# Optimization experiments

Measured on AMD Instinct MI355X. Metric: run time of the kernel, lower is better.

Reference implementation:

```python
import jax, jax.numpy as jnp
import numpy as np

N_TASK, N_WORKER, N_STATION = 20000, 5000, 1000
D, HEADS, LAYERS = 64, 4, 2
EDGE_COUNTS = [50000, 30000, 30000, 40000, 40000]
# (n_src, n_dst) per relation: precedes, assigned_to, has_task, can_do, done_by
EDGE_SPEC = [(N_TASK, N_TASK), (N_TASK, N_STATION), (N_STATION, N_TASK), (N_WORKER, N_TASK), (N_TASK, N_WORKER)]
EDGE_TYPES = [('task', 'task'), ('task', 'station'), ('station', 'task'), ('worker', 'task'), ('task', 'worker')]


def setup_inputs() -> dict:
    key = jax.random.key(0)
    ks = iter(jax.random.split(key, 64))
    inp = {}
    inp['x_task'] = jax.random.normal(next(ks), (N_TASK, 16), jnp.float32)
    inp['x_worker'] = jax.random.normal(next(ks), (N_WORKER, 12), jnp.float32)
    inp['x_station'] = jax.random.normal(next(ks), (N_STATION, 10), jnp.float32)
    for i, (E, (ns, nd)) in enumerate(zip(EDGE_COUNTS, EDGE_SPEC)):
        src = jax.random.randint(next(ks), (E,), 0, ns)
        dst = jax.random.randint(next(ks), (E,), 0, nd)
        inp[f'ei{i}'] = jnp.stack([src, dst]).astype(jnp.int32)
    def lin(k, i, o):
        return jax.random.normal(k, (i, o), jnp.float32) / np.float32(np.sqrt(i))
    # feature embedder params (Linear + LayerNorm affine) per node type
    for name, fd in [('task', 16), ('worker', 12), ('station', 10)]:
        inp[f'W_{name}'] = lin(next(ks), fd, D)
        inp[f'b_{name}'] = jnp.zeros((D,), jnp.float32)
        inp[f'g_{name}'] = jnp.ones((D,), jnp.float32)
        inp[f'beta_{name}'] = jnp.zeros((D,), jnp.float32)
    # stacked GATv2 params: [layers, 5 edge types, ...]
    inp['gat_Wl'] = jax.random.normal(next(ks), (LAYERS, 5, D, HEADS * D), jnp.float32) / np.float32(np.sqrt(D))
    inp['gat_Wr'] = jax.random.normal(next(ks), (LAYERS, 5, D, HEADS * D), jnp.float32) / np.float32(np.sqrt(D))
    inp['gat_att'] = jax.random.normal(next(ks), (LAYERS, 5, HEADS, D), jnp.float32) * np.float32(0.1)
    inp['gat_bias'] = jnp.zeros((LAYERS, 5, D), jnp.float32)
    return inp


def _layer_norm(x, g, b):
    m = x.mean(-1, keepdims=True)
    v = ((x - m) ** 2).mean(-1, keepdims=True)
    return (x - m) * jax.lax.rsqrt(v + 1e-5) * g + b


def _gatv2(x_src, x_dst, ei, Wl, Wr, att, bias):
    # GATv2Conv, concat=False (mean over heads), no self loops
    n_dst = x_dst.shape[0]
    xl = (x_src @ Wl).reshape(-1, HEADS, D)  # [Ns,H,Dh]
    xr = (x_dst @ Wr).reshape(-1, HEADS, D)  # [Nd,H,Dh]
    src, dst = ei[0], ei[1]
    e = jax.nn.leaky_relu(xl[src] + xr[dst], 0.2)          # [E,H,Dh]
    logits = jnp.einsum('ehd,hd->eh', e, att)              # [E,H]
    m = jax.ops.segment_max(logits, dst, num_segments=n_dst)
    ex = jnp.exp(logits - m[dst])
    denom = jax.ops.segment_sum(ex, dst, num_segments=n_dst)
    alpha = ex / denom[dst]                                # segment softmax per dst node
    out = jax.ops.segment_sum(alpha[..., None] * xl[src], dst, num_segments=n_dst)
    return out.mean(axis=1) + bias                         # [Nd,D]


def _forward(x_task, x_worker, x_station, eis,
             W_task, b_task, g_task, beta_task,
             W_worker, b_worker, g_worker, beta_worker,
             W_station, b_station, g_station, beta_station,
             gat_Wl, gat_Wr, gat_att, gat_bias):
    x = {
        'task': jax.nn.relu(_layer_norm(x_task @ W_task + b_task, g_task, beta_task)),
        'worker': jax.nn.relu(_layer_norm(x_worker @ W_worker + b_worker, g_worker, beta_worker)),
        'station': jax.nn.relu(_layer_norm(x_station @ W_station + b_station, g_station, beta_station)),
    }
    for l in range(LAYERS):
        agg = {'task': 0.0, 'worker': 0.0, 'station': 0.0}
        for t, (st, dt) in enumerate(EDGE_TYPES):
            agg[dt] = agg[dt] + _gatv2(x[st], x[dt], eis[t], gat_Wl[l, t], gat_Wr[l, t], gat_att[l, t], gat_bias[l, t])
        x = {k: jax.nn.relu(agg[k]) + x[k] for k in x}  # HeteroConv sum aggr, then ReLU + residual
    gc = jnp.concatenate([
        x['station'].mean(0), x['task'].mean(0), x['worker'].mean(0),
        x['station'].max(0), x['task'].max(0), x['worker'].max(0),
    ])[None, :]  # [1, 6*D]
    return x['task'], x['worker'], x['station'], gc


def reference(x_task, x_worker, x_station, ei0, ei1, ei2, ei3, ei4,
              W_task, b_task, g_task, beta_task,
              W_worker, b_worker, g_worker, beta_worker,
              W_station, b_station, g_station, beta_station,
              gat_Wl, gat_Wr, gat_att, gat_bias):
    return _forward(x_task, x_worker, x_station, (ei0, ei1, ei2, ei3, ei4),
                    W_task, b_task, g_task, beta_task,
                    W_worker, b_worker, g_worker, beta_worker,
                    W_station, b_station, g_station, beta_station,
                    gat_Wl, gat_Wr, gat_att, gat_bias)
```

## Files before the change

kernel.cpp:

```cpp
#include <hip/hip_runtime.h>
#include <math.h>

#define NT 20000
#define NW 5000
#define NS 1000

typedef __attribute__((ext_vector_type(8))) short bf16x8;
typedef __attribute__((ext_vector_type(4))) float f32x4;

#define CB_T 1250
#define CB_W 313
#define CB_S 63
#define CB_ALL 1626

struct GemmSeg { const short* X; const short* Wt; short* Y; int N; int blk0; };
struct GemmTab { GemmSeg s[10]; int nseg; };

struct GatTab {
  const int* rowp[5]; const int* col[5];
  const short* xl[5]; const short* xr[5];
  const float* att; const float* bias;
  float* aggT; float* aggW; float* aggS;
};

struct EdgeSeg { const int* ei; int* cnt; int* col; int E; int blk0; };
struct EdgeTab { EdgeSeg s[5]; int nseg; };

struct ScanTab { int* cnt[5]; int* rowp[5]; int n[5]; };

struct Mega0 {
  const float *xT, *xW, *xS, *WT, *WW, *WS;
  const float *bT, *gT, *beT, *bW, *gW, *beW, *bS, *gS, *beS;
  float *yT, *yW, *yS; short *ybT, *ybW, *ybS;
  const float *gWl, *gWr; short *Wlt, *Wrt; int* nxtAll;
};

__device__ __forceinline__ float wsum64(float v) {
  #pragma unroll
  for (int o = 32; o > 0; o >>= 1) v += __shfl_xor(v, o, 64);
  return v;
}
__device__ __forceinline__ short f2b(float f) {
  unsigned u = __float_as_uint(f);
  unsigned r = (u + 0x7FFFu + ((u >> 16) & 1u)) >> 16;
  return (short)(unsigned short)r;
}
__device__ __forceinline__ float blo(unsigned x) { return __uint_as_float(x << 16); }
__device__ __forceinline__ float bhi(unsigned x) { return __uint_as_float(x & 0xFFFF0000u); }

__global__ void mega0_kernel(Mega0 M) {
  int b = blockIdx.x;
  if (b < 6500) {
    int gid = b * 256 + threadIdx.x;
    int wid = gid >> 6, lane = gid & 63;
    const float *x, *W, *bb, *gg, *be; float* y; short* yb; int FD, n;
    if (wid < NT)            { x = M.xT; W = M.WT; bb = M.bT; gg = M.gT; be = M.beT; y = M.yT; yb = M.ybT; FD = 16; n = wid; }
    else if (wid < NT + NW)  { x = M.xW; W = M.WW; bb = M.bW; gg = M.gW; be = M.beW; y = M.yW; yb = M.ybW; FD = 12; n = wid - NT; }
    else                     { x = M.xS; W = M.WS; bb = M.bS; gg = M.gS; be = M.beS; y = M.yS; yb = M.ybS; FD = 10; n = wid - NT - NW; }
    const float* xr = x + (size_t)n * FD;
    float acc = bb[lane];
    for (int k = 0; k < FD; ++k) acc = fmaf(xr[k], W[k * 64 + lane], acc);
    float m = wsum64(acc) * (1.f / 64.f);
    float d = acc - m;
    float v = wsum64(d * d) * (1.f / 64.f);
    float o = d * rsqrtf(v + 1e-5f) * gg[lane] + be[lane];
    o = fmaxf(o, 0.f);
    y[(size_t)n * 64 + lane] = o;
    yb[(size_t)n * 64 + lane] = f2b(o);
  } else {
    int idx = (b - 6500) * 256 + threadIdx.x;
    if (idx < 66000) M.nxtAll[idx] = 0;
    int side = idx >= 163840;
    int j = idx - side * 163840;
    int m = j >> 14, e = j & 16383;
    int k = e >> 8, colv = e & 255;
    const float* src = side ? M.gWr : M.gWl;
    short* dst = side ? M.Wrt : M.Wlt;
    dst[m * 16384 + colv * 64 + k] = f2b(src[m * 16384 + e]);
  }
}

__global__ void count_kernel(EdgeTab tab) {
  int b = blockIdx.x, si = 0;
  for (int i = 1; i < tab.nseg; ++i) if (b >= tab.s[i].blk0) si = i;
  EdgeSeg sg = tab.s[si];
  int e = (b - sg.blk0) * 256 + threadIdx.x;
  if (e < sg.E) atomicAdd(&sg.cnt[sg.ei[sg.E + e]], 1);
}

__global__ void scan_kernel(ScanTab tab) {
  int t = blockIdx.x;
  int* cnt = tab.cnt[t]; int* rowp = tab.rowp[t]; int n = tab.n[t];
  __shared__ int wsums[16];
  __shared__ int carry_s;
  int tid = threadIdx.x, lane = tid & 63, w = tid >> 6;
  if (tid == 0) carry_s = 0;
  __syncthreads();
  for (int base = 0; base < n; base += 1024) {
    int i = base + tid;
    int v = (i < n) ? cnt[i] : 0;
    int s = v;
    #pragma unroll
    for (int o = 1; o < 64; o <<= 1) { int x = __shfl_up(s, o, 64); if (lane >= o) s += x; }
    if (lane == 63) wsums[w] = s;
    __syncthreads();
    if (w == 0 && lane < 16) {
      int x = wsums[lane];
      #pragma unroll
      for (int o = 1; o < 16; o <<= 1) { int y = __shfl_up(x, o, 16); if (lane >= o) x += y; }
      wsums[lane] = x;
    }
    __syncthreads();
    int carry   = carry_s;
    int waveoff = (w == 0) ? 0 : wsums[w - 1];
    int exc     = carry + waveoff + s - v;
    if (i < n) { rowp[i] = exc; cnt[i] = exc; }
    __syncthreads();
    if (tid == 0) carry_s += wsums[15];
    __syncthreads();
  }
  if (threadIdx.x == 0) rowp[n] = carry_s;
}

__global__ void fill_kernel(EdgeTab tab) {
  int b = blockIdx.x, si = 0;
  for (int i = 1; i < tab.nseg; ++i) if (b >= tab.s[i].blk0) si = i;
  EdgeSeg sg = tab.s[si];
  int e = (b - sg.blk0) * 256 + threadIdx.x;
  if (e >= sg.E) return;
  int s = sg.ei[e], d = sg.ei[sg.E + e];
  int pos = atomicAdd(&sg.cnt[d], 1);
  sg.col[pos] = s;
}

__global__ __launch_bounds__(256) void gemm_kernel(GemmTab tab) {
  __shared__ short lds[4096 + 16896];
  int b = blockIdx.x, si = 0;
  for (int i = 1; i < tab.nseg; ++i) if (b >= tab.s[i].blk0) si = i;
  GemmSeg sg = tab.s[si];
  int r0 = (b - sg.blk0) * 64;
  int tid = threadIdx.x;
  #pragma unroll
  for (int it = 0; it < 2; ++it) {
    int idx = it * 256 + tid;
    int row = idx >> 3, kq = idx & 7;
    bf16x8 v = {0, 0, 0, 0, 0, 0, 0, 0};
    if (r0 + row < sg.N) v = *(const bf16x8*)&sg.X[(size_t)(r0 + row) * 64 + kq * 8];
    *(bf16x8*)&lds[(row * 8 + (kq ^ (row & 7))) * 8] = v;
  }
  #pragma unroll
  for (int it = 0; it < 8; ++it) {
    int idx = it * 256 + tid;
    int col = idx >> 3, kq = idx & 7;
    bf16x8 v = *(const bf16x8*)&sg.Wt[col * 64 + kq * 8];
    *(bf16x8*)&lds[4096 + (col * 8 + (kq ^ (col & 7))) * 8] = v;
  }
  __syncthreads();
  int lane = tid & 63, wv = tid >> 6;
  int r = lane & 15, hk = lane >> 4;
  f32x4 acc[4][4];
  #pragma unroll
  for (int rt = 0; rt < 4; ++rt)
    #pragma unroll
    for (int ct = 0; ct < 4; ++ct) acc[rt][ct] = (f32x4){0.f, 0.f, 0.f, 0.f};
  #pragma unroll
  for (int kk = 0; kk < 2; ++kk) {
    int kq = kk * 4 + hk;
    bf16x8 a[4], bb[4];
    #pragma unroll
    for (int rt = 0; rt < 4; ++rt) {
      int row = rt * 16 + r;
      a[rt] = *(const bf16x8*)&lds[(row * 8 + (kq ^ (row & 7))) * 8];
    }
    #pragma unroll
    for (int ct = 0; ct < 4; ++ct) {
      int col = wv * 64 + ct * 16 + r;
      bb[ct] = *(const bf16x8*)&lds[4096 + (col * 8 + (kq ^ (col & 7))) * 8];
    }
    #pragma unroll
    for (int rt = 0; rt < 4; ++rt)
      #pragma unroll
      for (int ct = 0; ct < 4; ++ct)
        acc[rt][ct] = __builtin_amdgcn_mfma_f32_16x16x32_bf16(a[rt], bb[ct], acc[rt][ct], 0, 0, 0);
  }
  __syncthreads();
  #pragma unroll
  for (int rt = 0; rt < 4; ++rt)
    #pragma unroll
    for (int j = 0; j < 4; ++j) {
      int rowl = rt * 16 + hk * 4 + j;
      #pragma unroll
      for (int ct = 0; ct < 4; ++ct)
        lds[rowl * 264 + wv * 64 + ct * 16 + r] = f2b(acc[rt][ct][j]);
    }
  __syncthreads();
  #pragma unroll
  for (int it = 0; it < 8; ++it) {
    int idx = it * 256 + tid;
    int row = idx >> 5, v8 = idx & 31;
    if (r0 + row < sg.N) {
      bf16x8 v = *(const bf16x8*)&lds[row * 264 + v8 * 8];
      *(bf16x8*)&sg.Y[(size_t)(r0 + row) * 256 + v8 * 8] = v;
    }
  }
}

__global__ void gat_kernel(GatTab tab) {
  int gwave = (blockIdx.x * blockDim.x + threadIdx.x) >> 6;
  int lane  = threadIdx.x & 63;
  int h = lane >> 4, lig = lane & 15;
  int nrel, n; float* agg;
  int rels[3];
  if (gwave < NT)            { nrel = 3; rels[0] = 0; rels[1] = 2; rels[2] = 3; n = gwave; agg = tab.aggT; }
  else if (gwave < NT + NW)  { nrel = 1; rels[0] = 4; rels[1] = 4; rels[2] = 4; n = gwave - NT; agg = tab.aggW; }
  else if (gwave < NT + NW + NS) { nrel = 1; rels[0] = 1; rels[1] = 1; rels[2] = 1; n = gwave - NT - NW; agg = tab.aggS; }
  else return;
  float o0 = 0.f, o1 = 0.f, o2 = 0.f, o3 = 0.f;
  for (int ri = 0; ri < nrel; ++ri) {
    int r = rels[ri];
    int beg = tab.rowp[r][n], end = tab.rowp[r][n + 1];
    const short* xl = tab.xl[r];
    const int* colp = tab.col[r];
    uint2 xru = *(const uint2*)&tab.xr[r][(size_t)n * 256 + h * 64 + lig * 4];
    float4 a4 = *(const float4*)&tab.att[r * 256 + h * 64 + lig * 4];
    float xr0 = blo(xru.x), xr1 = bhi(xru.x), xr2 = blo(xru.y), xr3 = bhi(xru.y);
    if (end > beg) {
      float den = 0.f, c0 = 0.f, c1 = 0.f, c2 = 0.f, c3 = 0.f;
      int sNxt = colp[beg];
      uint2 w = *(const uint2*)&xl[(size_t)sNxt * 256 + h * 64 + lig * 4];
      if (beg + 1 < end) sNxt = colp[beg + 1];
      for (int i = beg; i < end; ++i) {
        uint2 wc = w;
        if (i + 1 < end) w = *(const uint2*)&xl[(size_t)sNxt * 256 + h * 64 + lig * 4];
        if (i + 2 < end) sNxt = colp[i + 2];
        float f0 = blo(wc.x), f1 = bhi(wc.x), f2v = blo(wc.y), f3 = bhi(wc.y);
        float vx = f0 + xr0, vy = f1 + xr1, vz = f2v + xr2, vw = f3 + xr3;
        vx = fmaxf(vx, 0.2f * vx); vy = fmaxf(vy, 0.2f * vy);
        vz = fmaxf(vz, 0.2f * vz); vw = fmaxf(vw, 0.2f * vw);
        float dd = fmaf(vx, a4.x, fmaf(vy, a4.y, fmaf(vz, a4.z, vw * a4.w)));
        dd += __shfl_xor(dd, 1, 64);
        dd += __shfl_xor(dd, 2, 64);
        dd += __shfl_xor(dd, 4, 64);
        dd += __shfl_xor(dd, 8, 64);
        float e = __expf(dd);
        den += e;
        c0 = fmaf(e, f0, c0); c1 = fmaf(e, f1, c1);
        c2 = fmaf(e, f2v, c2); c3 = fmaf(e, f3, c3);
      }
      float inv = 1.f / den;
      o0 = fmaf(c0, inv, o0); o1 = fmaf(c1, inv, o1);
      o2 = fmaf(c2, inv, o2); o3 = fmaf(c3, inv, o3);
    }
  }
  o0 += __shfl_xor(o0, 16, 64); o0 += __shfl_xor(o0, 32, 64);
  o1 += __shfl_xor(o1, 16, 64); o1 += __shfl_xor(o1, 32, 64);
  o2 += __shfl_xor(o2, 16, 64); o2 += __shfl_xor(o2, 32, 64);
  o3 += __shfl_xor(o3, 16, 64); o3 += __shfl_xor(o3, 32, 64);
  if (lane < 16) {
    float4 bs = make_float4(0.f, 0.f, 0.f, 0.f);
    for (int ri = 0; ri < nrel; ++ri) {
      float4 b4 = *(const float4*)&tab.bias[rels[ri] * 64 + lane * 4];
      bs.x += b4.x; bs.y += b4.y; bs.z += b4.z; bs.w += b4.w;
    }
    float4 res;
    res.x = fmaf(0.25f, o0, bs.x); res.y = fmaf(0.25f, o1, bs.y);
    res.z = fmaf(0.25f, o2, bs.z); res.w = fmaf(0.25f, o3, bs.w);
    *(float4*)&agg[(size_t)n * 64 + lane * 4] = res;
  }
}

template <int POOL>
__global__ __launch_bounds__(256) void combine_kernel(
    const float4* __restrict__ aT, const float4* __restrict__ aW, const float4* __restrict__ aS,
    const float4* __restrict__ xT, const float4* __restrict__ xW, const float4* __restrict__ xS,
    float4* __restrict__ oT, float4* __restrict__ oW, float4* __restrict__ oS,
    unsigned* __restrict__ bT, unsigned* __restrict__ bW, unsigned* __restrict__ bS,
    float4* __restrict__ psum, float4* __restrict__ pmax) {
  int b = blockIdx.x, tid = threadIdx.x;
  const float4 *a, *x; float4* o; unsigned* bo; int n4, local;
  if (b < CB_T)              { a = aT; x = xT; o = oT; bo = bT; n4 = NT * 16; local = b; }
  else if (b < CB_T + CB_W)  { a = aW; x = xW; o = oW; bo = bW; n4 = NW * 16; local = b - CB_T; }
  else                       { a = aS; x = xS; o = oS; bo = bS; n4 = NS * 16; local = b - CB_T - CB_W; }
  int j = local * 256 + tid;
  bool valid = j < n4;
  float4 r = make_float4(0.f, 0.f, 0.f, 0.f);
  if (valid) {
    float4 av = a[j], xv = x[j];
    r.x = fmaxf(av.x, 0.f) + xv.x; r.y = fmaxf(av.y, 0.f) + xv.y;
    r.z = fmaxf(av.z, 0.f) + xv.z; r.w = fmaxf(av.w, 0.f) + xv.w;
    o[j] = r;
    if (POOL == 0 && bo) {
      unsigned lo = (unsigned)(unsigned short)f2b(r.x) | ((unsigned)(unsigned short)f2b(r.y) << 16);
      unsigned hi = (unsigned)(unsigned short)f2b(r.z) | ((unsigned)(unsigned short)f2b(r.w) << 16);
      bo[j * 2] = lo; bo[j * 2 + 1] = hi;
    }
  }
  if (POOL) {
    float4 s = r;
    float4 m = valid ? r : make_float4(-3e38f, -3e38f, -3e38f, -3e38f);
    #pragma unroll
    for (int off = 16; off <= 32; off <<= 1) {
      s.x += __shfl_xor(s.x, off, 64); s.y += __shfl_xor(s.y, off, 64);
      s.z += __shfl_xor(s.z, off, 64); s.w += __shfl_xor(s.w, off, 64);
      m.x = fmaxf(m.x, __shfl_xor(m.x, off, 64)); m.y = fmaxf(m.y, __shfl_xor(m.y, off, 64));
      m.z = fmaxf(m.z, __shfl_xor(m.z, off, 64)); m.w = fmaxf(m.w, __shfl_xor(m.w, off, 64));
    }
    __shared__ float4 ls[4][16], lm[4][16];
    int w = tid >> 6, q = tid & 15;
    if (((tid >> 4) & 3) == 0) { ls[w][q] = s; lm[w][q] = m; }
    __syncthreads();
    if (tid < 16) {
      float4 S = ls[0][tid], M = lm[0][tid];
      #pragma unroll
      for (int i = 1; i < 4; ++i) {
        float4 s2 = ls[i][tid], m2 = lm[i][tid];
        S.x += s2.x; S.y += s2.y; S.z += s2.z; S.w += s2.w;
        M.x = fmaxf(M.x, m2.x); M.y = fmaxf(M.y, m2.y);
        M.z = fmaxf(M.z, m2.z); M.w = fmaxf(M.w, m2.w);
      }
      psum[b * 16 + tid] = S;
      pmax[b * 16 + tid] = M;
    }
  }
}

__global__ void pool2_kernel(const float* __restrict__ psum,
                             const float* __restrict__ pmax,
                             float* __restrict__ gc) {
  int b = blockIdx.x;
  int lane = threadIdx.x & 63, w = threadIdx.x >> 6;
  int off, cnt, N, mi;
  if (b == 0)      { off = CB_T + CB_W; cnt = CB_S; N = NS; mi = 0;   }
  else if (b == 1) { off = 0;           cnt = CB_T; N = NT; mi = 64;  }
  else             { off = CB_T;        cnt = CB_W; N = NW; mi = 128; }
  float s = 0.f, mx = -3e38f;
  for (int i = w; i < cnt; i += 16) {
    s += psum[(size_t)(off + i) * 64 + lane];
    mx = fmaxf(mx, pmax[(size_t)(off + i) * 64 + lane]);
  }
  __shared__ float ss[16][64], sm[16][64];
  ss[w][lane] = s; sm[w][lane] = mx;
  __syncthreads();
  if (w == 0) {
    #pragma unroll
    for (int i = 1; i < 16; ++i) { s += ss[i][lane]; mx = fmaxf(mx, sm[i][lane]); }
    gc[mi + lane] = s / (float)N;
    gc[192 + mi + lane] = mx;
  }
}

extern "C" void kernel_launch(void* const* d_in, const int* in_sizes, int n_in,
                              void* d_out, int out_size, void* d_ws, size_t ws_size,
                              hipStream_t stream) {
  const float* x_in[3] = {(const float*)d_in[0], (const float*)d_in[1], (const float*)d_in[2]};
  const int*   ei[5]   = {(const int*)d_in[3], (const int*)d_in[4], (const int*)d_in[5],
                          (const int*)d_in[6], (const int*)d_in[7]};
  const float* Wemb[3] = {(const float*)d_in[8],  (const float*)d_in[12], (const float*)d_in[16]};
  const float* bemb[3] = {(const float*)d_in[9],  (const float*)d_in[13], (const float*)d_in[17]};
  const float* gemb[3] = {(const float*)d_in[10], (const float*)d_in[14], (const float*)d_in[18]};
  const float* beemb[3]= {(const float*)d_in[11], (const float*)d_in[15], (const float*)d_in[19]};
  const float* gWl   = (const float*)d_in[20];
  const float* gWr   = (const float*)d_in[21];
  const float* gatt  = (const float*)d_in[22];
  const float* gbias = (const float*)d_in[23];

  const int NN[3]  = {NT, NW, NS};
  const int EC[5]  = {50000, 30000, 30000, 40000, 40000};
  const int STy[5] = {0, 0, 2, 1, 0};
  const int DTy[5] = {0, 2, 0, 0, 1};

  char* p = (char*)d_ws;
  auto alloc = [&](size_t bytes) -> void* {
    void* r = (void*)p;
    p += (bytes + 255) & ~(size_t)255;
    return r;
  };
  float* xc[3];  short* xcb[3];
  for (int k = 0; k < 3; ++k) xc[k]  = (float*)alloc((size_t)NN[k] * 64 * 4);
  for (int k = 0; k < 3; ++k) xcb[k] = (short*)alloc((size_t)NN[k] * 64 * 2);
  float* aggT = (float*)alloc((size_t)NT * 64 * 4);
  float* aggW = (float*)alloc((size_t)NW * 64 * 4);
  float* aggS = (float*)alloc((size_t)NS * 64 * 4);
  int* nxtAll = (int*)alloc((size_t)66000 * 4);
  int  nxtOff[5] = {0, NT, NT + NS, 2 * NT + NS, 3 * NT + NS};
  int* nxt[5]; for (int t = 0; t < 5; ++t) nxt[t] = nxtAll + nxtOff[t];
  int *rowp[5], *col[5];
  for (int t = 0; t < 5; ++t) {
    rowp[t] = (int*)alloc((size_t)(NN[DTy[t]] + 1) * 4);
    col[t]  = (int*)alloc((size_t)EC[t] * 4);
  }
  float* psum = (float*)alloc((size_t)CB_ALL * 64 * 4);
  float* pmax = (float*)alloc((size_t)CB_ALL * 64 * 4);
  short* Wlt  = (short*)alloc((size_t)10 * 16384 * 2);
  short* Wrt  = (short*)alloc((size_t)10 * 16384 * 2);
  short *xlT[5], *xrT[5];
  for (int t = 0; t < 5; ++t) {
    xlT[t] = (short*)alloc((size_t)NN[STy[t]] * 256 * 2);
    xrT[t] = (short*)alloc((size_t)NN[DTy[t]] * 256 * 2);
  }

  EdgeTab etab; etab.nseg = 5;
  int eb = 0;
  for (int t = 0; t < 5; ++t) {
    etab.s[t] = {ei[t], nxt[t], col[t], EC[t], eb};
    eb += (EC[t] + 255) / 256;
  }

  Mega0 M;
  M.xT = x_in[0]; M.xW = x_in[1]; M.xS = x_in[2];
  M.WT = Wemb[0]; M.WW = Wemb[1]; M.WS = Wemb[2];
  M.bT = bemb[0]; M.gT = gemb[0]; M.beT = beemb[0];
  M.bW = bemb[1]; M.gW = gemb[1]; M.beW = beemb[1];
  M.bS = bemb[2]; M.gS = gemb[2]; M.beS = beemb[2];
  M.yT = xc[0]; M.yW = xc[1]; M.yS = xc[2];
  M.ybT = xcb[0]; M.ybW = xcb[1]; M.ybS = xcb[2];
  M.gWl = gWl; M.gWr = gWr; M.Wlt = Wlt; M.Wrt = Wrt; M.nxtAll = nxtAll;
  mega0_kernel<<<7780, 256, 0, stream>>>(M);

  count_kernel<<<eb, 256, 0, stream>>>(etab);
  ScanTab stab;
  for (int t = 0; t < 5; ++t) { stab.cnt[t] = nxt[t]; stab.rowp[t] = rowp[t]; stab.n[t] = NN[DTy[t]]; }
  scan_kernel<<<5, 1024, 0, stream>>>(stab);
  fill_kernel<<<eb, 256, 0, stream>>>(etab);

  float* outT = (float*)d_out;
  float* outW = outT + (size_t)NT * 64;
  float* outS = outW + (size_t)NW * 64;
  float* gc   = outS + (size_t)NS * 64;

  for (int l = 0; l < 2; ++l) {
    GemmTab gt; gt.nseg = 10;
    int gb = 0;
    for (int t = 0; t < 5; ++t) {
      size_t off = (size_t)(l * 5 + t);
      gt.s[2 * t + 0] = {xcb[STy[t]], Wlt + off * 16384, xlT[t], NN[STy[t]], gb};
      gb += (NN[STy[t]] + 63) / 64;
      gt.s[2 * t + 1] = {xcb[DTy[t]], Wrt + off * 16384, xrT[t], NN[DTy[t]], gb};
      gb += (NN[DTy[t]] + 63) / 64;
    }
    gemm_kernel<<<gb, 256, 0, stream>>>(gt);

    GatTab at;
    for (int t = 0; t < 5; ++t) {
      at.rowp[t] = rowp[t]; at.col[t] = col[t];
      at.xl[t] = xlT[t]; at.xr[t] = xrT[t];
    }
    at.att  = gatt  + (size_t)l * 5 * 256;
    at.bias = gbias + (size_t)l * 5 * 64;
    at.aggT = aggT; at.aggW = aggW; at.aggS = aggS;
    gat_kernel<<<(26000 * 64 + 255) / 256, 256, 0, stream>>>(at);

    if (l == 0) {
      combine_kernel<0><<<CB_ALL, 256, 0, stream>>>(
          (const float4*)aggT, (const float4*)aggW, (const float4*)aggS,
          (const float4*)xc[0], (const float4*)xc[1], (const float4*)xc[2],
          (float4*)xc[0], (float4*)xc[1], (float4*)xc[2],
          (unsigned*)xcb[0], (unsigned*)xcb[1], (unsigned*)xcb[2],
          nullptr, nullptr);
    } else {
      combine_kernel<1><<<CB_ALL, 256, 0, stream>>>(
          (const float4*)aggT, (const float4*)aggW, (const float4*)aggS,
          (const float4*)xc[0], (const float4*)xc[1], (const float4*)xc[2],
          (float4*)outT, (float4*)outW, (float4*)outS,
          nullptr, nullptr, nullptr,
          (float4*)psum, (float4*)pmax);
    }
  }

  pool2_kernel<<<3, 1024, 0, stream>>>(psum, pmax, gc);
}
```

Measured before the change: 236.0 us.

## Split task GAT relations into separate waves and batch neighbor gathers

```diff
diff --git a/kernel.cpp b/kernel.cpp
--- a/kernel.cpp
+++ b/kernel.cpp
@@ -20,7 +20,7 @@
   const int* rowp[5]; const int* col[5];
   const short* xl[5]; const short* xr[5];
   const float* att; const float* bias;
-  float* aggT; float* aggW; float* aggS;
+  float* aggT0; float* aggT2; float* aggT3; float* aggW; float* aggS;
 };
 
 struct EdgeSeg { const int* ei; int* cnt; int* col; int E; int blk0; };
@@ -205,87 +205,108 @@
   }
 }
 
-__global__ void gat_kernel(GatTab tab) {
-  int gwave = (blockIdx.x * blockDim.x + threadIdx.x) >> 6;
-  int lane  = threadIdx.x & 63;
-  int h = lane >> 4, lig = lane & 15;
-  int nrel, n; float* agg;
-  int rels[3];
-  if (gwave < NT)            { nrel = 3; rels[0] = 0; rels[1] = 2; rels[2] = 3; n = gwave; agg = tab.aggT; }
-  else if (gwave < NT + NW)  { nrel = 1; rels[0] = 4; rels[1] = 4; rels[2] = 4; n = gwave - NT; agg = tab.aggW; }
-  else if (gwave < NT + NW + NS) { nrel = 1; rels[0] = 1; rels[1] = 1; rels[2] = 1; n = gwave - NT - NW; agg = tab.aggS; }
-  else return;
+template <int C>
+__device__ __forceinline__ void gat_node(const int* __restrict__ rowp,
+                                         const int* __restrict__ colp,
+                                         const short* __restrict__ xl,
+                                         const short* __restrict__ xr,
+                                         const float* __restrict__ att,
+                                         const float* __restrict__ bias,
+                                         float* __restrict__ agg,
+                                         int n, int lane, int h, int lig) {
+  int beg = rowp[n], end = rowp[n + 1];
+  uint2 xru = *(const uint2*)&xr[(size_t)n * 256 + h * 64 + lig * 4];
+  float4 a4 = *(const float4*)&att[h * 64 + lig * 4];
+  float xr0 = blo(xru.x), xr1 = bhi(xru.x), xr2 = blo(xru.y), xr3 = bhi(xru.y);
+  float den = 0.f, c0 = 0.f, c1 = 0.f, c2 = 0.f, c3 = 0.f;
+  for (int i0 = beg; i0 < end; i0 += C) {
+    uint2 w[C];
+    #pragma unroll
+    for (int k = 0; k < C; ++k) {
+      int c = colp[min(i0 + k, end - 1)];
+      w[k] = *(const uint2*)&xl[(size_t)c * 256 + h * 64 + lig * 4];
+    }
+    #pragma unroll
+    for (int k = 0; k < C; ++k) {
+      float f0 = blo(w[k].x), f1 = bhi(w[k].x), f2v = blo(w[k].y), f3 = bhi(w[k].y);
+      float vx = f0 + xr0, vy = f1 + xr1, vz = f2v + xr2, vw = f3 + xr3;
+      vx = fmaxf(vx, 0.2f * vx); vy = fmaxf(vy, 0.2f * vy);
+      vz = fmaxf(vz, 0.2f * vz); vw = fmaxf(vw, 0.2f * vw);
+      float dd = fmaf(vx, a4.x, fmaf(vy, a4.y, fmaf(vz, a4.z, vw * a4.w)));
+      dd += __shfl_xor(dd, 1, 64);
+      dd += __shfl_xor(dd, 2, 64);
+      dd += __shfl_xor(dd, 4, 64);
+      dd += __shfl_xor(dd, 8, 64);
+      float e = (i0 + k < end) ? __expf(dd) : 0.f;
+      den += e;
+      c0 = fmaf(e, f0, c0); c1 = fmaf(e, f1, c1);
+      c2 = fmaf(e, f2v, c2); c3 = fmaf(e, f3, c3);
+    }
+  }
   float o0 = 0.f, o1 = 0.f, o2 = 0.f, o3 = 0.f;
-  for (int ri = 0; ri < nrel; ++ri) {
-    int r = rels[ri];
-    int beg = tab.rowp[r][n], end = tab.rowp[r][n + 1];
-    const short* xl = tab.xl[r];
-    const int* colp = tab.col[r];
-    uint2 xru = *(const uint2*)&tab.xr[r][(size_t)n * 256 + h * 64 + lig * 4];
-    float4 a4 = *(const float4*)&tab.att[r * 256 + h * 64 + lig * 4];
-    float xr0 = blo(xru.x), xr1 = bhi(xru.x), xr2 = blo(xru.y), xr3 = bhi(xru.y);
-    if (end > beg) {
-      float den = 0.f, c0 = 0.f, c1 = 0.f, c2 = 0.f, c3 = 0.f;
-      int sNxt = colp[beg];
-      uint2 w = *(const uint2*)&xl[(size_t)sNxt * 256 + h * 64 + lig * 4];
-      if (beg + 1 < end) sNxt = colp[beg + 1];
-      for (int i = beg; i < end; ++i) {
-        uint2 wc = w;
-        if (i + 1 < end) w = *(const uint2*)&xl[(size_t)sNxt * 256 + h * 64 + lig * 4];
-        if (i + 2 < end) sNxt = colp[i + 2];
-        float f0 = blo(wc.x), f1 = bhi(wc.x), f2v = blo(wc.y), f3 = bhi(wc.y);
-        float vx = f0 + xr0, vy = f1 + xr1, vz = f2v + xr2, vw = f3 + xr3;
-        vx = fmaxf(vx, 0.2f * vx); vy = fmaxf(vy, 0.2f * vy);
-        vz = fmaxf(vz, 0.2f * vz); vw = fmaxf(vw, 0.2f * vw);
-        float dd = fmaf(vx, a4.x, fmaf(vy, a4.y, fmaf(vz, a4.z, vw * a4.w)));
-        dd += __shfl_xor(dd, 1, 64);
-        dd += __shfl_xor(dd, 2, 64);
-        dd += __shfl_xor(dd, 4, 64);
-        dd += __shfl_xor(dd, 8, 64);
-        float e = __expf(dd);
-        den += e;
-        c0 = fmaf(e, f0, c0); c1 = fmaf(e, f1, c1);
-        c2 = fmaf(e, f2v, c2); c3 = fmaf(e, f3, c3);
-      }
-      float inv = 1.f / den;
-      o0 = fmaf(c0, inv, o0); o1 = fmaf(c1, inv, o1);
-      o2 = fmaf(c2, inv, o2); o3 = fmaf(c3, inv, o3);
-    }
+  if (end > beg) {
+    float inv = 1.f / den;
+    o0 = c0 * inv; o1 = c1 * inv; o2 = c2 * inv; o3 = c3 * inv;
   }
   o0 += __shfl_xor(o0, 16, 64); o0 += __shfl_xor(o0, 32, 64);
   o1 += __shfl_xor(o1, 16, 64); o1 += __shfl_xor(o1, 32, 64);
   o2 += __shfl_xor(o2, 16, 64); o2 += __shfl_xor(o2, 32, 64);
   o3 += __shfl_xor(o3, 16, 64); o3 += __shfl_xor(o3, 32, 64);
   if (lane < 16) {
-    float4 bs = make_float4(0.f, 0.f, 0.f, 0.f);
-    for (int ri = 0; ri < nrel; ++ri) {
-      float4 b4 = *(const float4*)&tab.bias[rels[ri] * 64 + lane * 4];
-      bs.x += b4.x; bs.y += b4.y; bs.z += b4.z; bs.w += b4.w;
-    }
+    float4 b4 = *(const float4*)&bias[lane * 4];
     float4 res;
-    res.x = fmaf(0.25f, o0, bs.x); res.y = fmaf(0.25f, o1, bs.y);
-    res.z = fmaf(0.25f, o2, bs.z); res.w = fmaf(0.25f, o3, bs.w);
+    res.x = fmaf(0.25f, o0, b4.x); res.y = fmaf(0.25f, o1, b4.y);
+    res.z = fmaf(0.25f, o2, b4.z); res.w = fmaf(0.25f, o3, b4.w);
     *(float4*)&agg[(size_t)n * 64 + lane * 4] = res;
+  }
+}
+
+__global__ void gat_kernel(GatTab tab) {
+  int gwave = (blockIdx.x * blockDim.x + threadIdx.x) >> 6;
+  int lane  = threadIdx.x & 63;
+  int h = lane >> 4, lig = lane & 15;
+  if (gwave < 20000) {
+    gat_node<4>(tab.rowp[0], tab.col[0], tab.xl[0], tab.xr[0],
+                tab.att + 0 * 256, tab.bias + 0 * 64, tab.aggT0, gwave, lane, h, lig);
+  } else if (gwave < 40000) {
+    gat_node<4>(tab.rowp[2], tab.col[2], tab.xl[2], tab.xr[2],
+                tab.att + 2 * 256, tab.bias + 2 * 64, tab.aggT2, gwave - 20000, lane, h, lig);
+  } else if (gwave < 60000) {
+    gat_node<4>(tab.rowp[3], tab.col[3], tab.xl[3], tab.xr[3],
+                tab.att + 3 * 256, tab.bias + 3 * 64, tab.aggT3, gwave - 40000, lane, h, lig);
+  } else if (gwave < 65000) {
+    gat_node<8>(tab.rowp[4], tab.col[4], tab.xl[4], tab.xr[4],
+                tab.att + 4 * 256, tab.bias + 4 * 64, tab.aggW, gwave - 60000, lane, h, lig);
+  } else if (gwave < 66000) {
+    gat_node<8>(tab.rowp[1], tab.col[1], tab.xl[1], tab.xr[1],
+                tab.att + 1 * 256, tab.bias + 1 * 64, tab.aggS, gwave - 65000, lane, h, lig);
   }
 }
 
 template <int POOL>
 __global__ __launch_bounds__(256) void combine_kernel(
-    const float4* __restrict__ aT, const float4* __restrict__ aW, const float4* __restrict__ aS,
+    const float4* __restrict__ aT0, const float4* __restrict__ aT2, const float4* __restrict__ aT3,
+    const float4* __restrict__ aW, const float4* __restrict__ aS,
     const float4* __restrict__ xT, const float4* __restrict__ xW, const float4* __restrict__ xS,
     float4* __restrict__ oT, float4* __restrict__ oW, float4* __restrict__ oS,
     unsigned* __restrict__ bT, unsigned* __restrict__ bW, unsigned* __restrict__ bS,
     float4* __restrict__ psum, float4* __restrict__ pmax) {
   int b = blockIdx.x, tid = threadIdx.x;
-  const float4 *a, *x; float4* o; unsigned* bo; int n4, local;
-  if (b < CB_T)              { a = aT; x = xT; o = oT; bo = bT; n4 = NT * 16; local = b; }
+  const float4 *a, *x; float4* o; unsigned* bo; int n4, local; bool sum3 = false;
+  const float4 *a2 = nullptr, *a3 = nullptr;
+  if (b < CB_T)              { a = aT0; a2 = aT2; a3 = aT3; x = xT; o = oT; bo = bT; n4 = NT * 16; local = b; sum3 = true; }
   else if (b < CB_T + CB_W)  { a = aW; x = xW; o = oW; bo = bW; n4 = NW * 16; local = b - CB_T; }
   else                       { a = aS; x = xS; o = oS; bo = bS; n4 = NS * 16; local = b - CB_T - CB_W; }
   int j = local * 256 + tid;
   bool valid = j < n4;
   float4 r = make_float4(0.f, 0.f, 0.f, 0.f);
   if (valid) {
-    float4 av = a[j], xv = x[j];
+    float4 av = a[j];
+    if (sum3) {
+      float4 v2 = a2[j], v3 = a3[j];
+      av.x += v2.x + v3.x; av.y += v2.y + v3.y; av.z += v2.z + v3.z; av.w += v2.w + v3.w;
+    }
+    float4 xv = x[j];
     r.x = fmaxf(av.x, 0.f) + xv.x; r.y = fmaxf(av.y, 0.f) + xv.y;
     r.z = fmaxf(av.z, 0.f) + xv.z; r.w = fmaxf(av.w, 0.f) + xv.w;
     o[j] = r;
@@ -378,9 +399,11 @@
   float* xc[3];  short* xcb[3];
   for (int k = 0; k < 3; ++k) xc[k]  = (float*)alloc((size_t)NN[k] * 64 * 4);
   for (int k = 0; k < 3; ++k) xcb[k] = (short*)alloc((size_t)NN[k] * 64 * 2);
-  float* aggT = (float*)alloc((size_t)NT * 64 * 4);
-  float* aggW = (float*)alloc((size_t)NW * 64 * 4);
-  float* aggS = (float*)alloc((size_t)NS * 64 * 4);
+  float* aggT0 = (float*)alloc((size_t)NT * 64 * 4);
+  float* aggT2 = (float*)alloc((size_t)NT * 64 * 4);
+  float* aggT3 = (float*)alloc((size_t)NT * 64 * 4);
+  float* aggW  = (float*)alloc((size_t)NW * 64 * 4);
+  float* aggS  = (float*)alloc((size_t)NS * 64 * 4);
   int* nxtAll = (int*)alloc((size_t)66000 * 4);
   int  nxtOff[5] = {0, NT, NT + NS, 2 * NT + NS, 3 * NT + NS};
   int* nxt[5]; for (int t = 0; t < 5; ++t) nxt[t] = nxtAll + nxtOff[t];
@@ -447,19 +470,22 @@
     }
     at.att  = gatt  + (size_t)l * 5 * 256;
     at.bias = gbias + (size_t)l * 5 * 64;
-    at.aggT = aggT; at.aggW = aggW; at.aggS = aggS;
-    gat_kernel<<<(26000 * 64 + 255) / 256, 256, 0, stream>>>(at);
+    at.aggT0 = aggT0; at.aggT2 = aggT2; at.aggT3 = aggT3;
+    at.aggW = aggW; at.aggS = aggS;
+    gat_kernel<<<(66000 * 64) / 256, 256, 0, stream>>>(at);
 
     if (l == 0) {
       combine_kernel<0><<<CB_ALL, 256, 0, stream>>>(
-          (const float4*)aggT, (const float4*)aggW, (const float4*)aggS,
+          (const float4*)aggT0, (const float4*)aggT2, (const float4*)aggT3,
+          (const float4*)aggW, (const float4*)aggS,
           (const float4*)xc[0], (const float4*)xc[1], (const float4*)xc[2],
           (float4*)xc[0], (float4*)xc[1], (float4*)xc[2],
           (unsigned*)xcb[0], (unsigned*)xcb[1], (unsigned*)xcb[2],
           nullptr, nullptr);
     } else {
       combine_kernel<1><<<CB_ALL, 256, 0, stream>>>(
-          (const float4*)aggT, (const float4*)aggW, (const float4*)aggS,
+          (const float4*)aggT0, (const float4*)aggT2, (const float4*)aggT3,
+          (const float4*)aggW, (const float4*)aggS,
           (const float4*)xc[0], (const float4*)xc[1], (const float4*)xc[2],
           (float4*)outT, (float4*)outW, (float4*)outS,
           nullptr, nullptr, nullptr,
```

Measured after the change: 256.2 us. +8.6%, slower.
